# Performance work log

Measured on AMD Instinct MI355X. Metric: run time of the kernel, lower is better.

Reference implementation:

```python
import jax, jax.numpy as jnp
import numpy as np

B, T, E = 4, 2048, 1024
H = 16
QK_SQUEEZE = 2
S = E // QK_SQUEEZE          # squeeze_dim = 512
SHD = S // H                 # squeeze_head_dim = 32
HD = E // H                  # head_dim = 64
SCALING = SHD ** -0.5


def setup_inputs() -> dict:
    key = jax.random.key(0)
    ks = jax.random.split(key, 9)
    def w(k, shape, fan_in):
        return jax.random.normal(k, shape, jnp.float32) * (fan_in ** -0.5)
    return {
        "hidden_states": jax.random.normal(ks[0], (B, T, E), jnp.float32),
        "Wq": w(ks[1], (E, S), E), "bq": jnp.zeros((S,), jnp.float32),
        "Wk": w(ks[2], (E, S), E), "bk": jnp.zeros((S,), jnp.float32),
        "Wv": w(ks[3], (E, E), E), "bv": jnp.zeros((E,), jnp.float32),
        "Wo": w(ks[4], (E, E), E), "bo": jnp.zeros((E,), jnp.float32),
    }


def reference(hidden_states, Wq, bq, Wk, bk, Wv, bv, Wo, bo):
    # Projections; Q pre-scaled as in the torch module.
    q = ((hidden_states @ Wq + bq) * SCALING).reshape(B, T, H, SHD)
    k = (hidden_states @ Wk + bk).reshape(B, T, H, SHD)
    v = (hidden_states @ Wv + bv).reshape(B, T, H, HD)
    # [B, H, Tq, Tk] attention logits with squeezed head dim.
    attn = jnp.einsum("bqhd,bkhd->bhqk", q, k)
    p = jax.nn.softmax(attn, axis=-1)  # dropout p=0.0 -> identity
    out = jnp.einsum("bhqk,bkhd->bqhd", p, v).reshape(B, T, E)
    return out @ Wo + bo
```

## Files before the change

### kernel.cpp

```cpp
#include <hip/hip_runtime.h>
#include <stdint.h>


#define QSCALE (0.17677669529663687f * 1.4426950408889634f)

typedef __bf16 bf16x8 __attribute__((ext_vector_type(8)));
typedef float f32x4 __attribute__((ext_vector_type(4)));
typedef float f32x8 __attribute__((ext_vector_type(8)));
typedef float f32x16 __attribute__((ext_vector_type(16)));
typedef unsigned int u32x2 __attribute__((ext_vector_type(2)));
typedef unsigned int u32x4v __attribute__((ext_vector_type(4)));

static __device__ __forceinline__ unsigned short f2b(float f) {
  return __builtin_bit_cast(unsigned short, (__bf16)f);
}
static __device__ __forceinline__ unsigned int cvtpk(float lo, float hi) {
  unsigned int r;
  asm("v_cvt_pk_bf16_f32 %0, %1, %2" : "=v"(r) : "v"(lo), "v"(hi));
  return r;
}
static __device__ __forceinline__ void gl_lds16(const void* g, void* s) {
  __builtin_amdgcn_global_load_lds(
      (const __attribute__((address_space(1))) unsigned int*)(uintptr_t)g,
      (__attribute__((address_space(3))) unsigned int*)(uintptr_t)s, 16, 0, 0);
}
static __device__ __forceinline__ void pswap(unsigned int& a, unsigned int& b) {
#if __has_builtin(__builtin_amdgcn_permlane32_swap)
  u32x2 r = __builtin_amdgcn_permlane32_swap(a, b, false, false);
  a = r.x;
  b = r.y;
#else
  asm("v_permlane32_swap_b32 %0, %1" : "+v"(a), "+v"(b));
#endif
}

__global__ __launch_bounds__(256) void k_prep(
    const float* __restrict__ hs, const float* __restrict__ Wq,
    const float* __restrict__ bq, const float* __restrict__ Wk,
    const float* __restrict__ bk, const float* __restrict__ Wv,
    const float* __restrict__ bv, const float* __restrict__ Wo,
    const float* __restrict__ bo, unsigned short* __restrict__ hsb,
    unsigned short* __restrict__ wqkvT, unsigned short* __restrict__ woT,
    float* __restrict__ bqkv) {
  __shared__ float tile[64][65];
  const int blk = blockIdx.x;
  const int t = threadIdx.x;

  if (blk < 8192) {
    const int i = (blk * 256 + t) * 4;
    float4 v = *(const float4*)(hs + i);
    ushort4 u = make_ushort4(f2b(v.x), f2b(v.y), f2b(v.z), f2b(v.w));
    *(ushort4*)(hsb + i) = u;
  } else if (blk < 8960) {
    const float* W;
    unsigned short* WT;
    int N, rel;
    float scale;
    if (blk < 8320) {
      W = Wq; WT = wqkvT; N = 512; scale = QSCALE; rel = blk - 8192;
    } else if (blk < 8448) {
      W = Wk; WT = wqkvT + 512 * 1024; N = 512; scale = 1.0f; rel = blk - 8320;
    } else if (blk < 8704) {
      W = Wv; WT = wqkvT + 1024 * 1024; N = 1024; scale = 1.0f; rel = blk - 8448;
    } else {
      W = Wo; WT = woT; N = 1024; scale = 1.0f; rel = blk - 8704;
    }
    const int kt = rel & 15, nt = rel >> 4;
    const int k0 = kt * 64, n0 = nt * 64;
    {
      int kl = t >> 2, c = t & 3;
      const float* src = W + (size_t)(k0 + kl) * N + n0 + c * 16;
#pragma unroll
      for (int j = 0; j < 4; j++) {
        float4 v = *(const float4*)(src + j * 4);
        tile[kl][c * 16 + j * 4 + 0] = v.x;
        tile[kl][c * 16 + j * 4 + 1] = v.y;
        tile[kl][c * 16 + j * 4 + 2] = v.z;
        tile[kl][c * 16 + j * 4 + 3] = v.w;
      }
    }
    __syncthreads();
    {
      int nl = t >> 2, c2 = t & 3;
      unsigned short us[16];
#pragma unroll
      for (int j = 0; j < 16; j++) us[j] = f2b(tile[c2 * 16 + j][nl] * scale);
      uint4 a, b;
      a.x = (unsigned)us[0] | ((unsigned)us[1] << 16);
      a.y = (unsigned)us[2] | ((unsigned)us[3] << 16);
      a.z = (unsigned)us[4] | ((unsigned)us[5] << 16);
      a.w = (unsigned)us[6] | ((unsigned)us[7] << 16);
      b.x = (unsigned)us[8] | ((unsigned)us[9] << 16);
      b.y = (unsigned)us[10] | ((unsigned)us[11] << 16);
      b.z = (unsigned)us[12] | ((unsigned)us[13] << 16);
      b.w = (unsigned)us[14] | ((unsigned)us[15] << 16);
      unsigned short* dst = WT + (size_t)(n0 + nl) * 1024 + k0 + c2 * 16;
      *(uint4*)dst = a;
      *(uint4*)(dst + 8) = b;
    }
  } else {
    const int n = (blk - 8960) * 256 + t;
    float v;
    if (n < 512) v = bq[n] * QSCALE;
    else if (n < 1024) v = bk[n - 512];
    else v = bv[n - 1024];
    bqkv[n] = v;
  }
}

__global__ __launch_bounds__(512, 2) void k_gemm256qkv(
    const unsigned short* __restrict__ A, const unsigned short* __restrict__ BT,
    const float* __restrict__ bias,
    unsigned short* __restrict__ qo, unsigned short* __restrict__ ko,
    unsigned short* __restrict__ vo) {
  __shared__ alignas(128) char smem[131072];
  const int tid = threadIdx.x;
  const int w = tid >> 6, l = tid & 63, lm = l & 15, lc = l >> 4;
  const int wm = w >> 2, wn = w & 3;
  const int mt = blockIdx.x & 31, nt = blockIdx.x >> 5;
  const int brow = mt << 8, bcol = nt << 8;

  f32x4 acc[8][4] = {};

  auto stage = [&](int kt, int buf) {
    const unsigned short* As = A + (size_t)brow * 1024 + kt * 64;
    const unsigned short* Bs = BT + (size_t)bcol * 1024 + kt * 64;
    char* la = smem + buf * 32768;
    char* lb = smem + 65536 + buf * 32768;
#pragma unroll
    for (int j = 0; j < 4; j++) {
      const int p = j * 512 + tid;
      const int r = p >> 3;
      const int cc = (p & 7) ^ (r & 7);
      gl_lds16(As + (size_t)r * 1024 + cc * 8, la + (j * 512 + w * 64) * 16);
      gl_lds16(Bs + (size_t)r * 1024 + cc * 8, lb + (j * 512 + w * 64) * 16);
    }
  };

  stage(0, 0);
  stage(1, 1);
  asm volatile("s_waitcnt vmcnt(8)" ::: "memory");
  __builtin_amdgcn_s_barrier();
  __builtin_amdgcn_sched_barrier(0);

#pragma unroll 2
  for (int t = 0; t < 16; ++t) {
    const char* la = smem + (t & 1) * 32768;
    const char* lb = smem + 65536 + (t & 1) * 32768;
#pragma unroll
    for (int kk = 0; kk < 2; kk++) {
      const int csw = kk * 64 + lc * 16;
      bf16x8 af[8], bf[4];
#pragma unroll
      for (int mi = 0; mi < 8; mi++)
        af[mi] = *(const bf16x8*)(la + (wm * 128 + mi * 16 + lm) * 128 +
                                  (csw ^ ((lm & 7) << 4)));
#pragma unroll
      for (int ni = 0; ni < 4; ni++)
        bf[ni] = *(const bf16x8*)(lb + (wn * 64 + ni * 16 + lm) * 128 +
                                  (csw ^ ((lm & 7) << 4)));
      __builtin_amdgcn_s_setprio(1);
#pragma unroll
      for (int mi = 0; mi < 8; mi++)
#pragma unroll
        for (int ni = 0; ni < 4; ni++)
          acc[mi][ni] = __builtin_amdgcn_mfma_f32_16x16x32_bf16(af[mi], bf[ni],
                                                                acc[mi][ni], 0, 0, 0);
      __builtin_amdgcn_s_setprio(0);
    }
    asm volatile("s_waitcnt lgkmcnt(0)" ::: "memory");
    __builtin_amdgcn_sched_barrier(0);
    __builtin_amdgcn_s_barrier();
    if (t + 2 < 16) {
      stage(t + 2, t & 1);
      asm volatile("s_waitcnt vmcnt(8)" ::: "memory");
    } else {
      asm volatile("s_waitcnt vmcnt(0)" ::: "memory");
    }
    __builtin_amdgcn_s_barrier();
    __builtin_amdgcn_sched_barrier(0);
  }

#pragma unroll
  for (int nf = 0; nf < 4; nf++) {
    const int n = bcol + wn * 64 + nf * 16 + lm;
    const float bv_ = bias[n];
#pragma unroll
    for (int mf = 0; mf < 8; mf++) {
      const int m0 = brow + wm * 128 + mf * 16 + lc * 4;
      f32x4 v = acc[mf][nf];
      const float x0 = v[0] + bv_, x1 = v[1] + bv_, x2 = v[2] + bv_, x3 = v[3] + bv_;
      const int b = m0 >> 11, t0 = m0 & 2047;
      if (n < 1024) {
        unsigned short* dst = (n < 512) ? qo : ko;
        const int nn = n & 511, h = nn >> 5, d = nn & 31;
        const size_t base = ((size_t)((b << 4) + h) * 2048 + t0) * 32 + d;
        dst[base + 0 * 32] = f2b(x0);
        dst[base + 1 * 32] = f2b(x1);
        dst[base + 2 * 32] = f2b(x2);
        dst[base + 3 * 32] = f2b(x3);
      } else {
        const int e = n - 1024, h = e >> 6, hd = e & 63;
        ushort4 u = make_ushort4(f2b(x0), f2b(x1), f2b(x2), f2b(x3));
        *(ushort4*)(vo + (((size_t)((b << 4) + h) * 256 + (t0 >> 3)) * 64 + hd) * 8 +
                    (t0 & 7)) = u;
      }
    }
  }
}

__global__ __launch_bounds__(512, 2) void k_gemm256o(
    const unsigned short* __restrict__ A, const unsigned short* __restrict__ BT,
    const float* __restrict__ bias, float* __restrict__ fo) {
  __shared__ alignas(128) char smem[98304];
  const int tid = threadIdx.x;
  const int w = tid >> 6, l = tid & 63, lm = l & 15, lc = l >> 4;
  const int wm = w >> 2, wn = w & 3;
  const int mt = blockIdx.x & 31, nt = blockIdx.x >> 5;
  const int brow = mt << 8, bcol = nt << 7;

  f32x4 acc[8][2] = {};

  auto stage = [&](int kt, int buf) {
    const unsigned short* As = A + (size_t)brow * 1024 + kt * 64;
    const unsigned short* Bs = BT + (size_t)bcol * 1024 + kt * 64;
    char* la = smem + buf * 32768;
    char* lb = smem + 65536 + buf * 16384;
#pragma unroll
    for (int j = 0; j < 4; j++) {
      const int p = j * 512 + tid;
      const int r = p >> 3;
      const int cc = (p & 7) ^ (r & 7);
      gl_lds16(As + (size_t)r * 1024 + cc * 8, la + (j * 512 + w * 64) * 16);
    }
#pragma unroll
    for (int j = 0; j < 2; j++) {
      const int p = j * 512 + tid;
      const int r = p >> 3;
      const int cc = (p & 7) ^ (r & 7);
      gl_lds16(Bs + (size_t)r * 1024 + cc * 8, lb + (j * 512 + w * 64) * 16);
    }
  };

  stage(0, 0);
  stage(1, 1);
  asm volatile("s_waitcnt vmcnt(6)" ::: "memory");
  __builtin_amdgcn_s_barrier();
  __builtin_amdgcn_sched_barrier(0);

#pragma unroll 2
  for (int t = 0; t < 16; ++t) {
    const char* la = smem + (t & 1) * 32768;
    const char* lb = smem + 65536 + (t & 1) * 16384;
#pragma unroll
    for (int kk = 0; kk < 2; kk++) {
      const int csw = kk * 64 + lc * 16;
      bf16x8 af[8], bf[2];
#pragma unroll
      for (int mi = 0; mi < 8; mi++)
        af[mi] = *(const bf16x8*)(la + (wm * 128 + mi * 16 + lm) * 128 +
                                  (csw ^ ((lm & 7) << 4)));
#pragma unroll
      for (int ni = 0; ni < 2; ni++)
        bf[ni] = *(const bf16x8*)(lb + (wn * 32 + ni * 16 + lm) * 128 +
                                  (csw ^ ((lm & 7) << 4)));
      __builtin_amdgcn_s_setprio(1);
#pragma unroll
      for (int mi = 0; mi < 8; mi++)
#pragma unroll
        for (int ni = 0; ni < 2; ni++)
          acc[mi][ni] = __builtin_amdgcn_mfma_f32_16x16x32_bf16(af[mi], bf[ni],
                                                                acc[mi][ni], 0, 0, 0);
      __builtin_amdgcn_s_setprio(0);
    }
    asm volatile("s_waitcnt lgkmcnt(0)" ::: "memory");
    __builtin_amdgcn_sched_barrier(0);
    __builtin_amdgcn_s_barrier();
    if (t + 2 < 16) {
      stage(t + 2, t & 1);
      asm volatile("s_waitcnt vmcnt(6)" ::: "memory");
    } else {
      asm volatile("s_waitcnt vmcnt(0)" ::: "memory");
    }
    __builtin_amdgcn_s_barrier();
    __builtin_amdgcn_sched_barrier(0);
  }

#pragma unroll
  for (int nf = 0; nf < 2; nf++) {
    const int n = bcol + wn * 32 + nf * 16 + lm;
    const float bv_ = bias[n];
#pragma unroll
    for (int mf = 0; mf < 8; mf++) {
      const int m0 = brow + wm * 128 + mf * 16 + lc * 4;
      f32x4 v = acc[mf][nf];
      float* dst = fo + (size_t)m0 * 1024 + n;
      dst[0 * 1024] = v[0] + bv_;
      dst[1 * 1024] = v[1] + bv_;
      dst[2 * 1024] = v[2] + bv_;
      dst[3 * 1024] = v[3] + bv_;
    }
  }
}

__global__ __launch_bounds__(128, 3) void k_attn9(
    const unsigned short* __restrict__ qb, const unsigned short* __restrict__ kb,
    const unsigned short* __restrict__ v3, unsigned short* __restrict__ aout) {
  __shared__ float red[64][67];
  const int tid = threadIdx.x, kvh = tid >> 6, l = tid & 63;
  const int l31 = l & 31, hf = l >> 5;
  const int xcd = blockIdx.x & 7, slot = blockIdx.x >> 3;
  const int bh = xcd + ((slot >> 5) << 3);
  const int qrow0 = (slot & 31) << 6;

  const unsigned short* qrow = qb + ((size_t)bh * 2048 + qrow0 + l31) * 32 + hf * 8;
  const bf16x8 qA0 = *(const bf16x8*)(qrow);
  const bf16x8 qA1 = *(const bf16x8*)(qrow + 16);
  const bf16x8 qB0 = *(const bf16x8*)(qrow + 1024);
  const bf16x8 qB1 = *(const bf16x8*)(qrow + 1024 + 16);

  const unsigned short* kp = kb + ((size_t)bh * 2048 + kvh * 1024 + l31) * 32 + hf * 8;
  const unsigned short* vp = v3 + (((size_t)bh * 256 + kvh * 128 + hf) * 64 + l31) * 8;

  f32x16 oA0 = {}, oA1 = {}, oB0 = {}, oB1 = {};
  f32x4 lsA4 = {}, lsB4 = {};

  auto tile_body = [&](bf16x8 kf0, bf16x8 kf1, const unsigned short* vp_) {
    const bf16x8 va00 = *(const bf16x8*)(vp_ + 0);
    const bf16x8 va01 = *(const bf16x8*)(vp_ + 256);
    const bf16x8 va10 = *(const bf16x8*)(vp_ + 1024);
    const bf16x8 va11 = *(const bf16x8*)(vp_ + 1280);

    f32x16 sA = {}, sB = {};
    sA = __builtin_amdgcn_mfma_f32_32x32x16_bf16(kf0, qA0, sA, 0, 0, 0);
    sA = __builtin_amdgcn_mfma_f32_32x32x16_bf16(kf1, qA1, sA, 0, 0, 0);
    sB = __builtin_amdgcn_mfma_f32_32x32x16_bf16(kf0, qB0, sB, 0, 0, 0);
    sB = __builtin_amdgcn_mfma_f32_32x32x16_bf16(kf1, qB1, sB, 0, 0, 0);

#pragma unroll
    for (int i = 0; i < 16; i++) sA[i] = __builtin_amdgcn_exp2f(sA[i]);
#pragma unroll
    for (int i = 0; i < 16; i++) sB[i] = __builtin_amdgcn_exp2f(sB[i]);
    {
      f32x8 t8 = __builtin_shufflevector(sA, sA, 0, 1, 2, 3, 4, 5, 6, 7) +
                 __builtin_shufflevector(sA, sA, 8, 9, 10, 11, 12, 13, 14, 15);
      lsA4 += __builtin_shufflevector(t8, t8, 0, 1, 2, 3) +
              __builtin_shufflevector(t8, t8, 4, 5, 6, 7);
    }
    {
      f32x8 t8 = __builtin_shufflevector(sB, sB, 0, 1, 2, 3, 4, 5, 6, 7) +
                 __builtin_shufflevector(sB, sB, 8, 9, 10, 11, 12, 13, 14, 15);
      lsB4 += __builtin_shufflevector(t8, t8, 0, 1, 2, 3) +
              __builtin_shufflevector(t8, t8, 4, 5, 6, 7);
    }
    unsigned int pa[8], pb[8];
#pragma unroll
    for (int i = 0; i < 8; i++) pa[i] = cvtpk(sA[2 * i], sA[2 * i + 1]);
#pragma unroll
    for (int i = 0; i < 8; i++) pb[i] = cvtpk(sB[2 * i], sB[2 * i + 1]);
    pswap(pa[0], pa[2]);
    pswap(pa[1], pa[3]);
    pswap(pa[4], pa[6]);
    pswap(pa[5], pa[7]);
    pswap(pb[0], pb[2]);
    pswap(pb[1], pb[3]);
    pswap(pb[4], pb[6]);
    pswap(pb[5], pb[7]);
    const bf16x8 fA0 = __builtin_bit_cast(bf16x8, (u32x4v){pa[0], pa[1], pa[2], pa[3]});
    const bf16x8 fA1 = __builtin_bit_cast(bf16x8, (u32x4v){pa[4], pa[5], pa[6], pa[7]});
    const bf16x8 fB0 = __builtin_bit_cast(bf16x8, (u32x4v){pb[0], pb[1], pb[2], pb[3]});
    const bf16x8 fB1 = __builtin_bit_cast(bf16x8, (u32x4v){pb[4], pb[5], pb[6], pb[7]});

    __builtin_amdgcn_s_setprio(1);
    oA0 = __builtin_amdgcn_mfma_f32_32x32x16_bf16(va00, fA0, oA0, 0, 0, 0);
    oA1 = __builtin_amdgcn_mfma_f32_32x32x16_bf16(va01, fA0, oA1, 0, 0, 0);
    oB0 = __builtin_amdgcn_mfma_f32_32x32x16_bf16(va00, fB0, oB0, 0, 0, 0);
    oB1 = __builtin_amdgcn_mfma_f32_32x32x16_bf16(va01, fB0, oB1, 0, 0, 0);
    oA0 = __builtin_amdgcn_mfma_f32_32x32x16_bf16(va10, fA1, oA0, 0, 0, 0);
    oA1 = __builtin_amdgcn_mfma_f32_32x32x16_bf16(va11, fA1, oA1, 0, 0, 0);
    oB0 = __builtin_amdgcn_mfma_f32_32x32x16_bf16(va10, fB1, oB0, 0, 0, 0);
    oB1 = __builtin_amdgcn_mfma_f32_32x32x16_bf16(va11, fB1, oB1, 0, 0, 0);
    __builtin_amdgcn_s_setprio(0);
  };

  bf16x8 kf0 = *(const bf16x8*)(kp);
  bf16x8 kf1 = *(const bf16x8*)(kp + 16);

  for (int it = 0; it < 31; ++it) {
    kp += 1024;
    const bf16x8 nk0 = *(const bf16x8*)(kp);
    const bf16x8 nk1 = *(const bf16x8*)(kp + 16);

    tile_body(kf0, kf1, vp);
    vp += 2048;

    kf0 = nk0;
    kf1 = nk1;
  }
  tile_body(kf0, kf1, vp);

  float lsA = (lsA4[0] + lsA4[1]) + (lsA4[2] + lsA4[3]);
  float lsB = (lsB4[0] + lsB4[1]) + (lsB4[2] + lsB4[3]);
  lsA += __shfl_xor(lsA, 32);
  lsB += __shfl_xor(lsB, 32);

  if (kvh == 1) {
    float* r = &red[l][0];
#pragma unroll
    for (int i = 0; i < 16; i++) {
      r[i] = oA0[i];
      r[16 + i] = oA1[i];
      r[32 + i] = oB0[i];
      r[48 + i] = oB1[i];
    }
    r[64] = lsA;
    r[65] = lsB;
  }
  __syncthreads();
  if (kvh == 0) {
    const float* r = &red[l][0];
#pragma unroll
    for (int i = 0; i < 16; i++) {
      oA0[i] += r[i];
      oA1[i] += r[16 + i];
      oB0[i] += r[32 + i];
      oB1[i] += r[48 + i];
    }
    lsA += r[64];
    lsB += r[65];

    const int b = bh >> 4, hh = bh & 15;
    const float rA = 1.0f / lsA, rB = 1.0f / lsB;
    unsigned short* orowA = aout + ((size_t)(b * 2048 + qrow0 + l31)) * 1024 + hh * 64;
    unsigned short* orowB = orowA + (size_t)32 * 1024;
#pragma unroll
    for (int hc = 0; hc < 2; hc++) {
#pragma unroll
      for (int rg = 0; rg < 4; rg++) {
        const f32x16& oa = hc ? oA1 : oA0;
        ushort4 ua = make_ushort4(f2b(oa[rg * 4 + 0] * rA), f2b(oa[rg * 4 + 1] * rA),
                                  f2b(oa[rg * 4 + 2] * rA), f2b(oa[rg * 4 + 3] * rA));
        *(ushort4*)(orowA + hc * 32 + rg * 8 + hf * 4) = ua;
        const f32x16& ob = hc ? oB1 : oB0;
        ushort4 ub = make_ushort4(f2b(ob[rg * 4 + 0] * rB), f2b(ob[rg * 4 + 1] * rB),
                                  f2b(ob[rg * 4 + 2] * rB), f2b(ob[rg * 4 + 3] * rB));
        *(ushort4*)(orowB + hc * 32 + rg * 8 + hf * 4) = ub;
      }
    }
  }
}

extern "C" void kernel_launch(void* const* d_in, const int* in_sizes, int n_in,
                              void* d_out, int out_size, void* d_ws, size_t ws_size,
                              hipStream_t stream) {
  const float* hs = (const float*)d_in[0];
  const float* Wq = (const float*)d_in[1];
  const float* bq = (const float*)d_in[2];
  const float* Wk = (const float*)d_in[3];
  const float* bk = (const float*)d_in[4];
  const float* Wv = (const float*)d_in[5];
  const float* bv = (const float*)d_in[6];
  const float* Wo = (const float*)d_in[7];
  const float* bo = (const float*)d_in[8];

  char* ws = (char*)d_ws;
  unsigned short* hsb   = (unsigned short*)(ws + 0);
  unsigned short* wqkvT = (unsigned short*)(ws + 16777216);
  unsigned short* woT   = (unsigned short*)(ws + 20971520);
  float*          bqkv  = (float*)        (ws + 23068672);
  unsigned short* qbuf  = (unsigned short*)(ws + 23076864);
  unsigned short* kbuf  = (unsigned short*)(ws + 31465472);
  unsigned short* vTb   = (unsigned short*)(ws + 39854080);
  unsigned short* aoutb = (unsigned short*)(ws + 56631296);

  k_prep<<<8968, 256, 0, stream>>>(hs, Wq, bq, Wk, bk, Wv, bv, Wo, bo,
                                   hsb, wqkvT, woT, bqkv);
  k_gemm256qkv<<<256, 512, 0, stream>>>(hsb, wqkvT, bqkv, qbuf, kbuf, vTb);
  k_attn9<<<2048, 128, 0, stream>>>(qbuf, kbuf, vTb, aoutb);
  k_gemm256o<<<256, 512, 0, stream>>>(aoutb, woT, bo, (float*)d_out);
}
```

Before: 151.2 us.

## Software-pipeline attention QK MFMA one tile ahead of softmax and PV

Restructures the attention inner loop so the QK^T MFMAs for the next key tile are issued before the exp2/pack/PV work of the current tile, using double-buffered score registers in a 2x-unrolled loop. The goal is to overlap matrix-core work with the transcendental and VALU work and hide K/V load latency. The extra score buffers raise register pressure, so launch bounds drop from 3 to 2 waves-per-EU minimum, which may reduce occupancy.

```diff
diff --git a/kernel.cpp b/kernel.cpp
--- a/kernel.cpp
+++ b/kernel.cpp
@@ -303,7 +303,7 @@
   }
 }
 
-__global__ __launch_bounds__(128, 3) void k_attn9(
+__global__ __launch_bounds__(128, 2) void k_attn10(
     const unsigned short* __restrict__ qb, const unsigned short* __restrict__ kb,
     const unsigned short* __restrict__ v3, unsigned short* __restrict__ aout) {
   __shared__ float red[64][67];
@@ -325,18 +325,18 @@
   f32x16 oA0 = {}, oA1 = {}, oB0 = {}, oB1 = {};
   f32x4 lsA4 = {}, lsB4 = {};
 
-  auto tile_body = [&](bf16x8 kf0, bf16x8 kf1, const unsigned short* vp_) {
-    const bf16x8 va00 = *(const bf16x8*)(vp_ + 0);
-    const bf16x8 va01 = *(const bf16x8*)(vp_ + 256);
-    const bf16x8 va10 = *(const bf16x8*)(vp_ + 1024);
-    const bf16x8 va11 = *(const bf16x8*)(vp_ + 1280);
-
-    f32x16 sA = {}, sB = {};
-    sA = __builtin_amdgcn_mfma_f32_32x32x16_bf16(kf0, qA0, sA, 0, 0, 0);
-    sA = __builtin_amdgcn_mfma_f32_32x32x16_bf16(kf1, qA1, sA, 0, 0, 0);
-    sB = __builtin_amdgcn_mfma_f32_32x32x16_bf16(kf0, qB0, sB, 0, 0, 0);
-    sB = __builtin_amdgcn_mfma_f32_32x32x16_bf16(kf1, qB1, sB, 0, 0, 0);
-
+  auto qk_tile = [&](f32x16& sA, f32x16& sB, bf16x8 kf0, bf16x8 kf1) {
+    f32x16 a = {}, b = {};
+    a = __builtin_amdgcn_mfma_f32_32x32x16_bf16(kf0, qA0, a, 0, 0, 0);
+    a = __builtin_amdgcn_mfma_f32_32x32x16_bf16(kf1, qA1, a, 0, 0, 0);
+    b = __builtin_amdgcn_mfma_f32_32x32x16_bf16(kf0, qB0, b, 0, 0, 0);
+    b = __builtin_amdgcn_mfma_f32_32x32x16_bf16(kf1, qB1, b, 0, 0, 0);
+    sA = a;
+    sB = b;
+  };
+
+  auto finish_tile = [&](f32x16& sA, f32x16& sB, bf16x8 va00, bf16x8 va01, bf16x8 va10,
+                         bf16x8 va11) {
 #pragma unroll
     for (int i = 0; i < 16; i++) sA[i] = __builtin_amdgcn_exp2f(sA[i]);
 #pragma unroll
@@ -383,21 +383,38 @@
     __builtin_amdgcn_s_setprio(0);
   };
 
-  bf16x8 kf0 = *(const bf16x8*)(kp);
-  bf16x8 kf1 = *(const bf16x8*)(kp + 16);
-
-  for (int it = 0; it < 31; ++it) {
+  auto half = [&](f32x16& scA, f32x16& scB, f32x16& snA, f32x16& snB) {
+    const bf16x8 va00 = *(const bf16x8*)(vp + 0);
+    const bf16x8 va01 = *(const bf16x8*)(vp + 256);
+    const bf16x8 va10 = *(const bf16x8*)(vp + 1024);
+    const bf16x8 va11 = *(const bf16x8*)(vp + 1280);
+    vp += 2048;
     kp += 1024;
     const bf16x8 nk0 = *(const bf16x8*)(kp);
     const bf16x8 nk1 = *(const bf16x8*)(kp + 16);
-
-    tile_body(kf0, kf1, vp);
-    vp += 2048;
-
-    kf0 = nk0;
-    kf1 = nk1;
-  }
-  tile_body(kf0, kf1, vp);
+    qk_tile(snA, snB, nk0, nk1);
+    finish_tile(scA, scB, va00, va01, va10, va11);
+  };
+
+  f32x16 sA0, sB0, sA1, sB1;
+  {
+    const bf16x8 kf0 = *(const bf16x8*)(kp);
+    const bf16x8 kf1 = *(const bf16x8*)(kp + 16);
+    qk_tile(sA0, sB0, kf0, kf1);
+  }
+
+  for (int it = 0; it < 15; ++it) {
+    half(sA0, sB0, sA1, sB1);
+    half(sA1, sB1, sA0, sB0);
+  }
+  half(sA0, sB0, sA1, sB1);
+  {
+    const bf16x8 va00 = *(const bf16x8*)(vp + 0);
+    const bf16x8 va01 = *(const bf16x8*)(vp + 256);
+    const bf16x8 va10 = *(const bf16x8*)(vp + 1024);
+    const bf16x8 va11 = *(const bf16x8*)(vp + 1280);
+    finish_tile(sA1, sB1, va00, va01, va10, va11);
+  }
 
   float lsA = (lsA4[0] + lsA4[1]) + (lsA4[2] + lsA4[3]);
   float lsB = (lsB4[0] + lsB4[1]) + (lsB4[2] + lsB4[3]);
@@ -476,6 +493,6 @@
   k_prep<<<8968, 256, 0, stream>>>(hs, Wq, bq, Wk, bk, Wv, bv, Wo, bo,
                                    hsb, wqkvT, woT, bqkv);
   k_gemm256qkv<<<256, 512, 0, stream>>>(hsb, wqkvT, bqkv, qbuf, kbuf, vTb);
-  k_attn9<<<2048, 128, 0, stream>>>(qbuf, kbuf, vTb, aoutb);
+  k_attn10<<<2048, 128, 0, stream>>>(qbuf, kbuf, vTb, aoutb);
   k_gemm256o<<<256, 512, 0, stream>>>(aoutb, woT, bo, (float*)d_out);
 }
```

Result: faster. 142.3 us (-5.9%).
